# Performance work log

Hardware: AMD Instinct MI355X
Metric: run time of the kernel (lower is better)

Reference implementation:

```python
import math
import jax, jax.numpy as jnp
import numpy as np

N_TOKENS = 32768
N_TYPES = 21
D_MODEL = 1024
N_SEQS = 64


def setup_inputs() -> dict:
    key = jax.random.key(0)
    k1, k2, k3, k4 = jax.random.split(key, 4)
    x = jax.random.normal(k1, (N_TOKENS, N_TYPES), dtype=jnp.float32)
    # nn.Linear(n_types, d_model): weight [d_model, n_types], bias [d_model]
    W = jax.random.normal(k2, (D_MODEL, N_TYPES), dtype=jnp.float32) / math.sqrt(N_TYPES)
    b = jax.random.normal(k3, (D_MODEL,), dtype=jnp.float32) * 0.01
    # sorted segment ids -> ragged batch of N_SEQS sequences
    batch = jnp.sort(jax.random.randint(k4, (N_TOKENS,), 0, N_SEQS, dtype=jnp.int64))
    return {"x": x, "W": W, "b": b, "batch": batch}


def _position_encoding(max_len, d_model, dtype):
    pos = jnp.arange(max_len, dtype=jnp.float32)[:, None]          # [L,1]
    div = jnp.exp(jnp.arange(0, d_model, 2, dtype=jnp.float32) * (-math.log(10000.0) / d_model))
    ang = pos * div                                                 # [L, d/2]
    pe = jnp.zeros((max_len, d_model), dtype=jnp.float32)
    pe = pe.at[:, 0::2].set(jnp.sin(ang)).at[:, 1::2].set(jnp.cos(ang))
    return pe.astype(dtype)


def reference(x, W, b, batch):
    d_model = W.shape[0]
    # Linear projection + sqrt(d_model) scale
    h = (jnp.einsum('nt,dt->nd', x, W) + b) * math.sqrt(d_model)    # [N, d_model]

    # pad_batch: relabel via unique ids, compute per-token position within its
    # sequence, and scatter into a padded [n_seqs, max_len, d_model] tensor.
    bnp = np.asarray(batch)
    _, inv, counts = np.unique(bnp, return_inverse=True, return_counts=True)
    n_seqs = counts.shape[0]
    max_len = int(counts.max())
    offsets = np.concatenate([np.zeros(1, dtype=np.int64), np.cumsum(counts)[:-1]])
    pos = np.arange(bnp.shape[0], dtype=np.int64) - offsets[inv]    # position within sequence

    padded = jnp.zeros((n_seqs, max_len, d_model), dtype=h.dtype)
    padded = padded.at[jnp.asarray(inv), jnp.asarray(pos)].set(h)

    # mask: True where valid token (original returns ~pad_mask)
    mask = jnp.arange(max_len)[None, :] < jnp.asarray(counts)[:, None]

    pe = _position_encoding(max_len, d_model, h.dtype)              # [L, d_model]
    out = padded + pe[None, :, :]
    return (out, mask)
```

## Files before the change

kernel.cpp:

```cpp
#include <hip/hip_runtime.h>
#include <hip/hip_bf16.h>
#include <math.h>

#define RPB 26

typedef float f4 __attribute__((ext_vector_type(4)));

__global__ __launch_bounds__(1024) void setup_kernel(const int* __restrict__ batch,
                                                     int n, int* __restrict__ tables) {
  __shared__ int samp[256];
  __shared__ int csum[64];
  __shared__ int fine[64];
  __shared__ int sbase[64];
  __shared__ int lbs[65];
  __shared__ int stride_s;
  int t = threadIdx.x;
  if (t == 0) stride_s = (batch[n - 1] == 0) ? 2 : 1;
  if (t < 64) { csum[t] = 0; fine[t] = 0; }
  __syncthreads();
  int stride = stride_s;
  int window = (n + 255) >> 8;
  if (t < 256) {
    long long idx = (long long)t * window;
    if (idx > n - 1) idx = n - 1;
    samp[t] = batch[idx * stride];
  }
  __syncthreads();
  {
    int v = t >> 4, q = t & 15;
    int c = 0;
#pragma unroll
    for (int i = 0; i < 16; ++i) c += (samp[q * 16 + i] < v) ? 1 : 0;
    atomicAdd(&csum[v], c);
  }
  __syncthreads();
  if (t < 64) {
    int c = csum[t];
    sbase[t] = (c == 0) ? 0 : (c - 1) * window;
  }
  __syncthreads();
  {
    int v = t >> 4, q = t & 15;
    int wpt = (window + 15) >> 4;
    int S = sbase[v];
    int c = 0;
    for (int j = q * wpt; j < (q + 1) * wpt && j < window; ++j) {
      int idx = S + j;
      if (idx < n && batch[idx * stride] < v) c++;
    }
    atomicAdd(&fine[v], c);
  }
  __syncthreads();
  if (t < 64) {
    lbs[t] = sbase[t] + fine[t];
    if (t == 0) lbs[64] = n;
  }
  __syncthreads();
  if (t < 64) {
    int cnt = lbs[t + 1] - lbs[t];
    unsigned long long present = __ballot(cnt > 0);
    int seg = __popcll(present & ((1ull << t) - 1ull));
    int nseq = __popcll(present);
    if (cnt > 0) { tables[seg] = lbs[t]; tables[64 + seg] = cnt; }
    if (t >= nseq) { tables[t] = 0; tables[64 + t] = 0; }
  }
}

__global__ __launch_bounds__(256) void embed_kernel(
    const float* __restrict__ x, const float* __restrict__ W,
    const float* __restrict__ b, const int* __restrict__ tables,
    float* __restrict__ out, float* __restrict__ mask,
    int L, int totalRows) {
  int t = threadIdx.x;

  float wf[84];
  {
    const f4* wp = (const f4*)(W + 84 * t);
#pragma unroll
    for (int k = 0; k < 21; ++k) {
      f4 v = wp[k];
      wf[4 * k] = v[0]; wf[4 * k + 1] = v[1]; wf[4 * k + 2] = v[2]; wf[4 * k + 3] = v[3];
    }
  }
  f4 bb = *(const f4*)(b + 4 * t);

  __shared__ float xs[RPB][21];
  __shared__ int r_tok[RPB];
  __shared__ int r_p[RPB];

  int base = blockIdx.x * RPB;
  if (t < RPB) {
    int row = base + t;
    int tok = -1, p = 0;
    if (row < totalRows) {
      int s = row / L;
      p = row - s * L;
      int cnt = tables[64 + s];
      if (p < cnt) tok = tables[s] + p;
    }
    r_tok[t] = tok;
    r_p[t] = p;
  }
  __syncthreads();
  for (int u = t; u < RPB * 21; u += 256) {
    int rr = u / 21, k = u - rr * 21;
    int tok = r_tok[rr];
    if (tok >= 0) xs[rr][k] = x[tok * 21 + k];
  }
  __syncthreads();

  const float KC = -0.01798894603901599f;
  float divA = __expf(KC * (float)(2 * t));
  float divB = __expf(KC * (float)(2 * t + 1));

  float* po = out + (size_t)base * 1024 + 4 * t;
  for (int rr = 0; rr < RPB; ++rr) {
    int row = base + rr;
    if (row >= totalRows) break;
    float fp = (float)r_p[rr];
    float s0, c0, s1, c1;
    __sincosf(fp * divA, &s0, &c0);
    __sincosf(fp * divB, &s1, &c1);
    f4 res;
    int tok = r_tok[rr];
    if (tok >= 0) {
      float a0 = bb[0], a1 = bb[1], a2 = bb[2], a3 = bb[3];
#pragma unroll
      for (int k = 0; k < 21; ++k) {
        float xv = xs[rr][k];
        a0 = fmaf(xv, wf[k], a0);
        a1 = fmaf(xv, wf[21 + k], a1);
        a2 = fmaf(xv, wf[42 + k], a2);
        a3 = fmaf(xv, wf[63 + k], a3);
      }
      res[0] = fmaf(a0, 32.f, s0);
      res[1] = fmaf(a1, 32.f, c0);
      res[2] = fmaf(a2, 32.f, s1);
      res[3] = fmaf(a3, 32.f, c1);
    } else {
      res[0] = s0; res[1] = c0; res[2] = s1; res[3] = c1;
    }
    __builtin_nontemporal_store(res, (f4*)po);
    po += 1024;
  }

  if (t < RPB) {
    int row = base + t;
    if (row < totalRows) mask[row] = (r_tok[t] >= 0) ? 1.0f : 0.0f;
  }
}

extern "C" void kernel_launch(void* const* d_in, const int* in_sizes, int n_in,
                              void* d_out, int out_size, void* d_ws, size_t ws_size,
                              hipStream_t stream) {
  const float* x = (const float*)d_in[0];
  const float* W = (const float*)d_in[1];
  const float* b = (const float*)d_in[2];
  const int* batch = (const int*)d_in[3];
  int n_tokens = in_sizes[3];
  float* out = (float*)d_out;

  int L = out_size / (64 * 1025);
  int totalRows = 64 * L;

  int* tables = (int*)d_ws;

  setup_kernel<<<1, 1024, 0, stream>>>(batch, n_tokens, tables);
  int grid = (totalRows + RPB - 1) / RPB;
  embed_kernel<<<grid, 256, 0, stream>>>(x, W, b, tables, out,
                                         out + (size_t)totalRows * 1024,
                                         L, totalRows);
}
```

Baseline: 48.90 us.

## Drop shared-memory staging; advance positional encoding by rotation recurrence

Removes the shared-memory x staging and the two barriers. Each row now reads x through wave-uniform scalar loads (readfirstlane) and computes position and token indices incrementally. Per-row sincos is replaced by an angle-addition rotation recurrence seeded once per block, and stores become regular instead of nontemporal. It also adds launch_bounds occupancy 4 and fully unrolls the row loop, which risks register pressure and accumulated floating-point drift in the sin/cos recurrence over up to 26 steps.

```diff
diff --git a/kernel.cpp b/kernel.cpp
--- a/kernel.cpp
+++ b/kernel.cpp
@@ -66,87 +66,89 @@
   }
 }
 
-__global__ __launch_bounds__(256) void embed_kernel(
+__global__ __launch_bounds__(256, 4) void embed_kernel(
     const float* __restrict__ x, const float* __restrict__ W,
     const float* __restrict__ b, const int* __restrict__ tables,
     float* __restrict__ out, float* __restrict__ mask,
     int L, int totalRows) {
   int t = threadIdx.x;
 
-  float wf[84];
+  float arr[84];
   {
     const f4* wp = (const f4*)(W + 84 * t);
 #pragma unroll
     for (int k = 0; k < 21; ++k) {
       f4 v = wp[k];
-      wf[4 * k] = v[0]; wf[4 * k + 1] = v[1]; wf[4 * k + 2] = v[2]; wf[4 * k + 3] = v[3];
+      arr[4 * k] = v[0]; arr[4 * k + 1] = v[1]; arr[4 * k + 2] = v[2]; arr[4 * k + 3] = v[3];
     }
   }
-  f4 bb = *(const f4*)(b + 4 * t);
-
-  __shared__ float xs[RPB][21];
-  __shared__ int r_tok[RPB];
-  __shared__ int r_p[RPB];
+  f4 wv[21];
+#pragma unroll
+  for (int k = 0; k < 21; ++k) {
+    f4 v;
+    v[0] = arr[k]; v[1] = arr[21 + k]; v[2] = arr[42 + k]; v[3] = arr[63 + k];
+    wv[k] = v;
+  }
+  f4 bbv = *(const f4*)(b + 4 * t);
 
   int base = blockIdx.x * RPB;
-  if (t < RPB) {
-    int row = base + t;
-    int tok = -1, p = 0;
-    if (row < totalRows) {
-      int s = row / L;
-      p = row - s * L;
-      int cnt = tables[64 + s];
-      if (p < cnt) tok = tables[s] + p;
-    }
-    r_tok[t] = tok;
-    r_p[t] = p;
-  }
-  __syncthreads();
-  for (int u = t; u < RPB * 21; u += 256) {
-    int rr = u / 21, k = u - rr * 21;
-    int tok = r_tok[rr];
-    if (tok >= 0) xs[rr][k] = x[tok * 21 + k];
-  }
-  __syncthreads();
+  int s = base / L;
+  int p = base - s * L;
+  int st = tables[s];
+  int cnt = tables[64 + s];
 
   const float KC = -0.01798894603901599f;
   float divA = __expf(KC * (float)(2 * t));
   float divB = __expf(KC * (float)(2 * t + 1));
+  float sA, cA, sB, cB, dsA, dcA, dsB, dcB;
+  __sincosf((float)p * divA, &sA, &cA);
+  __sincosf((float)p * divB, &sB, &cB);
+  __sincosf(divA, &dsA, &dcA);
+  __sincosf(divB, &dsB, &dcB);
 
   float* po = out + (size_t)base * 1024 + 4 * t;
+#pragma unroll
   for (int rr = 0; rr < RPB; ++rr) {
     int row = base + rr;
     if (row >= totalRows) break;
-    float fp = (float)r_p[rr];
-    float s0, c0, s1, c1;
-    __sincosf(fp * divA, &s0, &c0);
-    __sincosf(fp * divB, &s1, &c1);
+
+    bool valid = (p < cnt);
+    int tok = valid ? st + p : 0;
+    int tok21 = __builtin_amdgcn_readfirstlane(tok * 21);
+    const float* xr = x + tok21;
+
+    float xk[21];
+#pragma unroll
+    for (int k = 0; k < 21; ++k) xk[k] = xr[k];
+
+    f4 pev; pev[0] = sA; pev[1] = cA; pev[2] = sB; pev[3] = cB;
     f4 res;
-    int tok = r_tok[rr];
-    if (tok >= 0) {
-      float a0 = bb[0], a1 = bb[1], a2 = bb[2], a3 = bb[3];
+    if (valid) {
+      f4 acc = bbv;
 #pragma unroll
-      for (int k = 0; k < 21; ++k) {
-        float xv = xs[rr][k];
-        a0 = fmaf(xv, wf[k], a0);
-        a1 = fmaf(xv, wf[21 + k], a1);
-        a2 = fmaf(xv, wf[42 + k], a2);
-        a3 = fmaf(xv, wf[63 + k], a3);
+      for (int k = 0; k < 21; ++k) acc += xk[k] * wv[k];
+      res = acc * 32.f + pev;
+    } else {
+      res = pev;
+    }
+    *(f4*)po = res;
+    po += 1024;
+    if (t == 0) mask[row] = valid ? 1.0f : 0.0f;
+
+    if (rr < RPB - 1) {
+      ++p;
+      if (p == L) {
+        p = 0; ++s;
+        st = tables[s]; cnt = tables[64 + s];
+        sA = 0.f; cA = 1.f; sB = 0.f; cB = 1.f;
+      } else {
+        float nsA = fmaf(sA, dcA, cA * dsA);
+        float ncA = fmaf(cA, dcA, -sA * dsA);
+        float nsB = fmaf(sB, dcB, cB * dsB);
+        float ncB = fmaf(cB, dcB, -sB * dsB);
+        sA = nsA; cA = ncA; sB = nsB; cB = ncB;
       }
-      res[0] = fmaf(a0, 32.f, s0);
-      res[1] = fmaf(a1, 32.f, c0);
-      res[2] = fmaf(a2, 32.f, s1);
-      res[3] = fmaf(a3, 32.f, c1);
-    } else {
-      res[0] = s0; res[1] = c0; res[2] = s1; res[3] = c1;
     }
-    __builtin_nontemporal_store(res, (f4*)po);
-    po += 1024;
-  }
-
-  if (t < RPB) {
-    int row = base + t;
-    if (row < totalRows) mask[row] = (r_tok[t] >= 0) ? 1.0f : 0.0f;
   }
 }
 
```

New measurement: 55.63 us. 13.8% more time.
